# Performance work log

Measured on AMD Instinct MI355X. Metric: run time of the kernel, lower is better.

## Reference

```python
import jax, jax.numpy as jnp
import numpy as np

B, T, C = 4, 2048, 2048
H = 16
D = C // H  # 128


def setup_inputs() -> dict:
    key = jax.random.key(0)
    k1, k2, k3, k4 = jax.random.split(key, 4)
    x = jax.random.normal(k1, (B, T, C), dtype=jnp.float32)
    rope_freqs = jax.random.uniform(k2, (D // 2,), dtype=jnp.float32)
    # torch Linear weights: (out_features, in_features)
    W_attn = jax.random.normal(k3, (3 * C, C), dtype=jnp.float32) * (1.0 / np.sqrt(C))
    W_proj = jax.random.normal(k4, (C, C), dtype=jnp.float32) * (1.0 / np.sqrt(C))
    return {"x": x, "rope_freqs": rope_freqs, "W_attn": W_attn, "W_proj": W_proj}


def _apply_rope(q, k, rope_freqs):
    # q, k: (B, H, T, D); rope_freqs: (D//2,)
    S = q.shape[2]
    positions = jnp.arange(S, dtype=q.dtype)[:, None]            # (S, 1)
    theta = positions * rope_freqs[None, :]                       # (S, D//2)
    sin_t = jnp.sin(theta)[None, None]                            # (1,1,S,D//2)
    cos_t = jnp.cos(theta)[None, None]
    q1, q2 = q[..., 0::2], q[..., 1::2]
    k1, k2 = k[..., 0::2], k[..., 1::2]
    q_out = jnp.concatenate([q1 * cos_t - q2 * sin_t, q1 * sin_t + q2 * cos_t], axis=-1)
    k_out = jnp.concatenate([k1 * cos_t - k2 * sin_t, k1 * sin_t + k2 * cos_t], axis=-1)
    return q_out, k_out


def reference(x, rope_freqs, W_attn, W_proj):
    b, t, c = x.shape
    qkv = jnp.einsum('btc,fc->btf', x, W_attn)                    # (B,T,3C)
    q, k, v = jnp.split(qkv, 3, axis=-1)
    q = q.reshape(b, t, H, D).transpose(0, 2, 1, 3)               # (B,H,T,D)
    k = k.reshape(b, t, H, D).transpose(0, 2, 1, 3)
    v = v.reshape(b, t, H, D).transpose(0, 2, 1, 3)
    q, k = _apply_rope(q, k, rope_freqs)
    scale = 1.0 / jnp.sqrt(jnp.asarray(D, dtype=x.dtype))
    scores = jnp.einsum('bhqd,bhkd->bhqk', q, k) * scale          # (B,H,T,T)
    causal = jnp.tril(jnp.ones((t, t), dtype=bool))
    scores = jnp.where(causal[None, None], scores, jnp.asarray(-jnp.inf, dtype=scores.dtype))
    probs = jax.nn.softmax(scores, axis=-1)
    y = jnp.einsum('bhqk,bhkd->bhqd', probs, v)                   # (B,H,T,D)
    y = y.transpose(0, 2, 1, 3).reshape(b, t, c)
    return jnp.einsum('btc,fc->btf', y, W_proj)
```

## Files before the change

### kernel.cpp

```cpp
#include <hip/hip_runtime.h>
#include <cstdint>
#include <cstddef>


typedef unsigned short u16;
typedef u16    u16x8 __attribute__((ext_vector_type(8)));
typedef __bf16 bf16x8 __attribute__((ext_vector_type(8)));
typedef float  f32x4 __attribute__((ext_vector_type(4)));

#define MFMA16(a, b, c) __builtin_amdgcn_mfma_f32_16x16x32_bf16( \
    __builtin_bit_cast(bf16x8, (a)), __builtin_bit_cast(bf16x8, (b)), (c), 0, 0, 0)

static __device__ __forceinline__ u16 f2b(float f) {
  unsigned u = __builtin_bit_cast(unsigned, f);
  unsigned r = (u + 0x7FFFu + ((u >> 16) & 1u)) >> 16;
  return (u16)r;
}

static __device__ __forceinline__ void gld_lds16(const void* g, void* l) {
  __builtin_amdgcn_global_load_lds(
      (__attribute__((address_space(1))) unsigned int*)(void*)(g),
      (__attribute__((address_space(3))) unsigned int*)(l),
      16, 0, 0);
}

#define BARRIER() asm volatile("s_barrier" ::: "memory")
#define LGKM0()   do { asm volatile("s_waitcnt lgkmcnt(0)" ::: "memory"); \
                       __builtin_amdgcn_sched_barrier(0); } while (0)
#define WAIT_VM(n) asm volatile("s_waitcnt vmcnt(" #n ")" ::: "memory")

__global__ __launch_bounds__(256) void cvt_bf16(const float4* __restrict__ src,
                                                u16x8* __restrict__ dst, int n8) {
  int i = blockIdx.x * 256 + threadIdx.x;
  if (i >= n8) return;
  float4 a = src[i * 2], b = src[i * 2 + 1];
  u16x8 o;
  o[0] = f2b(a.x); o[1] = f2b(a.y); o[2] = f2b(a.z); o[3] = f2b(a.w);
  o[4] = f2b(b.x); o[5] = f2b(b.y); o[6] = f2b(b.z); o[7] = f2b(b.w);
  dst[i] = o;
}

static __device__ __forceinline__ void rdA(u16x8 (&af)[4][2], const u16* p,
                                           int cx0, int cx1) {
#pragma unroll
  for (int i = 0; i < 4; ++i) {
    af[i][0] = *(const u16x8*)(p + i * 1024 + cx0);
    af[i][1] = *(const u16x8*)(p + i * 1024 + cx1);
  }
}

static __device__ __forceinline__ void rdB(u16x8 (&bf)[2][2], const u16* p,
                                           int cx0, int cx1) {
#pragma unroll
  for (int j = 0; j < 2; ++j) {
    bf[j][0] = *(const u16x8*)(p + j * 1024 + cx0);
    bf[j][1] = *(const u16x8*)(p + j * 1024 + cx1);
  }
}

static __device__ __forceinline__ void mm16(f32x4 (&acc)[8][4], int ib, int jb,
                                            const u16x8 (&af)[4][2],
                                            const u16x8 (&bf)[2][2]) {
#pragma unroll
  for (int i = 0; i < 4; ++i)
#pragma unroll
    for (int j = 0; j < 2; ++j) {
      acc[ib + i][jb + j] = MFMA16(af[i][0], bf[j][0], acc[ib + i][jb + j]);
      acc[ib + i][jb + j] = MFMA16(af[i][1], bf[j][1], acc[ib + i][jb + j]);
    }
}

static __device__ __forceinline__ void gemm256_main(
    const u16* __restrict__ A, const u16* __restrict__ Bw, int K,
    int m0, int n0, u16* sm, f32x4 (&acc)[8][4]) {
  const int tid = threadIdx.x;
  const int lane = tid & 63, wv = tid >> 6;
  const int quad = lane >> 4, col = lane & 15;
  const int wm = wv >> 2, wn = wv & 3;

  u16* LA0 = sm;
  u16* LB0 = sm + 16384;
  u16* LA1 = sm + 32768;
  u16* LB1 = sm + 49152;

#pragma unroll
  for (int i = 0; i < 8; ++i)
#pragma unroll
    for (int j = 0; j < 4; ++j) acc[i][j] = (f32x4){0.f, 0.f, 0.f, 0.f};

  const int r8 = lane >> 3, ch = lane & 7;
  const int sc8 = (ch ^ r8) << 3;
  const u16 *aS[4], *bS[4];
  int dof[4];
#pragma unroll
  for (int u = 0; u < 4; ++u) {
    int row = u * 64 + wv * 8 + r8;
    aS[u] = A + (size_t)(m0 + row) * K + sc8;
    bS[u] = Bw + (size_t)(n0 + row) * K + sc8;
    dof[u] = (u * 64 + wv * 8) * 64;
  }

  const int cx0 = ((quad) ^ (col & 7)) << 3;
  const int cx1 = ((4 | quad) ^ (col & 7)) << 3;
  const int offA = (wm * 128 + col) * 64;
  const int offB = (wn * 64 + col) * 64;

  gld_lds16(bS[0], LB0 + dof[0]); gld_lds16(bS[1], LB0 + dof[1]);
  gld_lds16(bS[2], LB0 + dof[2]); gld_lds16(bS[3], LB0 + dof[3]);
  gld_lds16(aS[0], LA0 + dof[0]); gld_lds16(aS[2], LA0 + dof[2]);
  gld_lds16(aS[1], LA0 + dof[1]); gld_lds16(aS[3], LA0 + dof[3]);
  WAIT_VM(2);
  BARRIER();

  u16x8 af[4][2], bfL[2][2], bfH[2][2];
  const int nIt = K >> 7;
#pragma unroll 1
  for (int it = 0; it < nIt; ++it) {
    const size_t ko = (size_t)it * 128 + 64;
    const size_t kn = (size_t)it * 128 + 128;
    const bool hn = (it + 1 < nIt);

    rdA(af, LA0 + offA, cx0, cx1);
    rdB(bfL, LB0 + offB, cx0, cx1);
    gld_lds16(bS[0] + ko, LB1 + dof[0]); gld_lds16(bS[1] + ko, LB1 + dof[1]);
    BARRIER(); LGKM0();
    __builtin_amdgcn_s_setprio(1); mm16(acc, 0, 0, af, bfL);
    __builtin_amdgcn_s_setprio(0);
    BARRIER();
    rdB(bfH, LB0 + offB + 2048, cx0, cx1);
    gld_lds16(bS[2] + ko, LB1 + dof[2]); gld_lds16(bS[3] + ko, LB1 + dof[3]);
    WAIT_VM(4);
    BARRIER(); LGKM0();
    __builtin_amdgcn_s_setprio(1); mm16(acc, 0, 2, af, bfH);
    __builtin_amdgcn_s_setprio(0);
    BARRIER();
    rdA(af, LA0 + offA + 4096, cx0, cx1);
    gld_lds16(aS[0] + ko, LA1 + dof[0]); gld_lds16(aS[2] + ko, LA1 + dof[2]);
    BARRIER(); LGKM0();
    __builtin_amdgcn_s_setprio(1); mm16(acc, 4, 0, af, bfL);
    __builtin_amdgcn_s_setprio(0);
    BARRIER();
    gld_lds16(aS[1] + ko, LA1 + dof[1]); gld_lds16(aS[3] + ko, LA1 + dof[3]);
    WAIT_VM(2);
    BARRIER(); __builtin_amdgcn_sched_barrier(0);
    __builtin_amdgcn_s_setprio(1); mm16(acc, 4, 2, af, bfH);
    __builtin_amdgcn_s_setprio(0);
    BARRIER();
    rdA(af, LA1 + offA, cx0, cx1);
    rdB(bfL, LB1 + offB, cx0, cx1);
    if (hn) { gld_lds16(bS[0] + kn, LB0 + dof[0]); gld_lds16(bS[1] + kn, LB0 + dof[1]); }
    BARRIER(); LGKM0();
    __builtin_amdgcn_s_setprio(1); mm16(acc, 0, 0, af, bfL);
    __builtin_amdgcn_s_setprio(0);
    BARRIER();
    rdB(bfH, LB1 + offB + 2048, cx0, cx1);
    if (hn) {
      gld_lds16(bS[2] + kn, LB0 + dof[2]); gld_lds16(bS[3] + kn, LB0 + dof[3]);
      WAIT_VM(4);
    } else {
      WAIT_VM(0);
    }
    BARRIER(); LGKM0();
    __builtin_amdgcn_s_setprio(1); mm16(acc, 0, 2, af, bfH);
    __builtin_amdgcn_s_setprio(0);
    BARRIER();
    rdA(af, LA1 + offA + 4096, cx0, cx1);
    if (hn) { gld_lds16(aS[0] + kn, LA0 + dof[0]); gld_lds16(aS[2] + kn, LA0 + dof[2]); }
    BARRIER(); LGKM0();
    __builtin_amdgcn_s_setprio(1); mm16(acc, 4, 0, af, bfL);
    __builtin_amdgcn_s_setprio(0);
    BARRIER();
    if (hn) { gld_lds16(aS[1] + kn, LA0 + dof[1]); gld_lds16(aS[3] + kn, LA0 + dof[3]); }
    WAIT_VM(2);
    BARRIER(); __builtin_amdgcn_sched_barrier(0);
    __builtin_amdgcn_s_setprio(1); mm16(acc, 4, 2, af, bfH);
    __builtin_amdgcn_s_setprio(0);
    BARRIER();
  }
}

__global__ __launch_bounds__(512, 2) void gemm_qkv(
    const u16* __restrict__ A, const u16* __restrict__ Bw,
    const float* __restrict__ freqs, int K,
    u16* __restrict__ Qp, u16* __restrict__ Kp, u16* __restrict__ Vp) {
  extern __shared__ u16 sm[];
  const int bid = blockIdx.x;
  const int x = bid & 7, o = bid >> 3;
  const int rnd = o >> 5, w = o & 31;
  const int m0 = (x * 4 + (w & 3)) * 256;
  const int n0 = (rnd * 8 + (w >> 2)) * 256;

  f32x4 acc[8][4];
  gemm256_main(A, Bw, K, m0, n0, sm, acc);

  const int tid = threadIdx.x;
  const int lane = tid & 63, wv = tid >> 6;
  const int quad = lane >> 4, col = lane & 15;
  const int wm = wv >> 2, wn = wv & 3;

  const int which = n0 >> 11;
  const int h0 = (n0 & 2047) >> 7;
  const int b = m0 >> 11, t0 = m0 & 2047;
  const int hl = wn >> 1;


  if (which == 2) {
#pragma unroll
    for (int j = 0; j < 4; ++j) {
      int d = (wn & 1) * 64 + j * 16 + col;
      int key = (d >> 1) & 7;
#pragma unroll
      for (int i = 0; i < 8; ++i) {
        int tbase = wm * 128 + i * 16 + quad * 4;
        int reg = hl * 4 + (tbase >> 6);
        int tc0 = tbase & 63;
        u16* d0 = sm + reg * 8192 + d * 64 + ((((tc0 >> 3) ^ key)) << 3) + (tc0 & 7);
        *(unsigned*)d0 = (unsigned)f2b(acc[i][j][0]) |
                         ((unsigned)f2b(acc[i][j][1]) << 16);
        *(unsigned*)(d0 + 2) = (unsigned)f2b(acc[i][j][2]) |
                               ((unsigned)f2b(acc[i][j][3]) << 16);
      }
    }
    __syncthreads();
#pragma unroll
    for (int s = 0; s < 16; ++s) {
      int cch = tid + (s << 9);
      int reg = cch >> 10, ci = cch & 1023;
      int d = ci >> 3, cc = ci & 7;
      u16x8 v = *(const u16x8*)(sm + reg * 8192 + d * 64 +
                                (((cc ^ ((d >> 1) & 7))) << 3));
      int hh = reg >> 2, ktg = reg & 3;
      int kt = (t0 >> 6) + ktg;
      size_t off = (((size_t)((b * 16 + h0 + hh) * 32 + kt)) << 13) +
                   (size_t)d * 64 + (cc << 3);
      *(u16x8*)(Vp + off) = v;
    }
  } else {
    u16* dst = (which == 0) ? Qp : Kp;
    const bool evenlane = (col & 1) == 0;
    const int rlo = evenlane ? 0 : 2;
#pragma unroll
    for (int j = 0; j < 4; ++j) {
      int dd = (wn & 1) * 64 + j * 16 + col;
      int jj = dd >> 1;
      float fr = freqs[jj];
#pragma unroll
      for (int i = 0; i < 8; ++i) {
        float oth[4];
#pragma unroll
        for (int r = 0; r < 4; ++r) oth[r] = __shfl_xor(acc[i][j][r], 1);
#pragma unroll
        for (int rr = 0; rr < 2; ++rr) {
          int r = rlo + rr;
          float q1 = evenlane ? acc[i][j][r] : oth[r];
          float q2 = evenlane ? oth[r] : acc[i][j][r];
          int tgl = wm * 128 + i * 16 + quad * 4 + r;
          int t = t0 + tgl;
          float theta = (float)t * fr;
          float rev = theta * 0.15915494309189535f;
          rev -= floorf(rev);
          float sn = __builtin_amdgcn_sinf(rev);
          float cs = __builtin_amdgcn_cosf(rev);
          unsigned pk = (unsigned)f2b(q1 * cs - q2 * sn) |
                        ((unsigned)f2b(q1 * sn + q2 * cs) << 16);
          int row = hl * 256 + tgl;
          int sc = (jj >> 2) ^ (row & 15);
          *(unsigned*)(sm + row * 128 + (sc << 3) + 2 * (jj & 3)) = pk;
        }
      }
    }
    __syncthreads();
#pragma unroll
    for (int s = 0; s < 16; ++s) {
      int cch = tid + (s << 9);
      int row = cch >> 4, cc = cch & 15;
      u16x8 v = *(const u16x8*)(sm + row * 128 + ((cc ^ (row & 15)) << 3));
      int hh = row >> 8, tl = row & 255;
      size_t off = ((size_t)((b * 16 + h0 + hh) * 2048 + t0 + tl)) * 128 +
                   (cc << 3);
      *(u16x8*)(dst + off) = v;
    }
  }
}

__global__ __launch_bounds__(512, 2) void gemm_proj(
    const u16* __restrict__ A, const u16* __restrict__ Bw,
    int N, int K, float* __restrict__ out) {
  extern __shared__ u16 sm[];
  const int m0 = blockIdx.y * 256, n0 = blockIdx.x * 256;

  f32x4 acc[8][4];
  gemm256_main(A, Bw, K, m0, n0, sm, acc);

  const int tid = threadIdx.x;
  const int lane = tid & 63, wv = tid >> 6;
  const int quad = lane >> 4, col = lane & 15;
  const int wm = wv >> 2, wn = wv & 3;

#pragma unroll
  for (int i = 0; i < 8; ++i) {
    int mg = m0 + wm * 128 + i * 16 + quad * 4;
#pragma unroll
    for (int j = 0; j < 4; ++j) {
      int ng = n0 + wn * 64 + j * 16 + col;
#pragma unroll
      for (int r = 0; r < 4; ++r) out[(size_t)(mg + r) * N + ng] = acc[i][j][r];
    }
  }
}

__global__ __launch_bounds__(512, 4) void fattn(
    const u16* __restrict__ Qb, const u16* __restrict__ Kb, const u16* __restrict__ Vt,
    u16* __restrict__ Yb) {
  __shared__ alignas(16) u16 lK[64 * 128];
  __shared__ alignas(16) u16 lVt[128 * 64];
  __shared__ alignas(16) u16 lP[8][16 * 64];

  const int tid = threadIdx.x;
  const int lane = tid & 63, wv = tid >> 6;
  const int quad = lane >> 4, col = lane & 15;
  const int bh = blockIdx.x;
  const int p = blockIdx.y;
  const int b = bh >> 4, h = bh & 15;
  const size_t base = (size_t)bh << 18;
  const float kcomb = 0.08838834764831845f * 1.4426950408889634f;

#pragma unroll 1
  for (int phase = 0; phase < 2; ++phase) {
    const int tq = phase ? (15 - p) : p;
    const int qr0 = tq * 128 + wv * 16;
    const int dkt = qr0 >> 6;

    u16x8 qf[4];
#pragma unroll
    for (int t = 0; t < 4; ++t)
      qf[t] = *(const u16x8*)(Qb + base + (size_t)(qr0 + col) * 128 + t * 32 + quad * 8);

    f32x4 mrow = (f32x4){-1e30f, -1e30f, -1e30f, -1e30f};
    f32x4 lrow = (f32x4){0.f, 0.f, 0.f, 0.f};
    f32x4 o[8];
#pragma unroll
    for (int dt = 0; dt < 8; ++dt) o[dt] = (f32x4){0.f, 0.f, 0.f, 0.f};

    const int nkt = 2 * tq + 2;
#pragma unroll 1
    for (int kt = 0; kt < nkt; ++kt) {
      __syncthreads();
      if (wv < 4) {
#pragma unroll
        for (int u = 0; u < 4; ++u) {
          int row = wv * 16 + u * 4 + (lane >> 4);
          int sc = (lane & 15) ^ (row & 15);
          gld_lds16(Kb + base + (size_t)(kt * 64 + row) * 128 + (sc << 3),
                    lK + (size_t)(wv * 16 + u * 4) * 128);
        }
      } else {
        int vw = wv - 4;
        const u16* vbase = Vt + ((size_t)(bh * 32 + kt) << 13);
#pragma unroll
        for (int u = 0; u < 4; ++u) {
          int row = vw * 32 + u * 8 + (lane >> 3);
          int sc = (lane & 7) ^ (row & 7);
          gld_lds16(vbase + (size_t)row * 64 + (sc << 3),
                    lVt + (size_t)(vw * 32 + u * 8) * 64);
        }
      }
      __syncthreads();

      if (kt <= dkt) {
        f32x4 sv[4];
#pragma unroll
        for (int nt = 0; nt < 4; ++nt) {
          f32x4 s = (f32x4){0.f, 0.f, 0.f, 0.f};
#pragma unroll
          for (int t = 0; t < 4; ++t) {
            int krow = nt * 16 + col;
            u16x8 kf = *(const u16x8*)&lK[krow * 128 + ((((t << 2) | quad) ^ (krow & 15)) << 3)];
            s = MFMA16(qf[t], kf, s);
          }
          sv[nt] = s;
        }
#pragma unroll
        for (int nt = 0; nt < 4; ++nt)
#pragma unroll
          for (int r = 0; r < 4; ++r) sv[nt][r] *= kcomb;
        if (kt == dkt) {
#pragma unroll
          for (int nt = 0; nt < 4; ++nt) {
            int cg = kt * 64 + nt * 16 + col;
#pragma unroll
            for (int r = 0; r < 4; ++r)
              if (cg > qr0 + quad * 4 + r) sv[nt][r] = -1e30f;
          }
        }
        f32x4 mx = sv[0];
#pragma unroll
        for (int nt = 1; nt < 4; ++nt)
#pragma unroll
          for (int r = 0; r < 4; ++r) mx[r] = fmaxf(mx[r], sv[nt][r]);
#pragma unroll
        for (int off = 1; off < 16; off <<= 1)
#pragma unroll
          for (int r = 0; r < 4; ++r) mx[r] = fmaxf(mx[r], __shfl_xor(mx[r], off));
        f32x4 alpha;
#pragma unroll
        for (int r = 0; r < 4; ++r) {
          float mn = fmaxf(mrow[r], mx[r]);
          alpha[r] = exp2f(mrow[r] - mn);
          mrow[r] = mn;
        }
        f32x4 ps = (f32x4){0.f, 0.f, 0.f, 0.f};
#pragma unroll
        for (int nt = 0; nt < 4; ++nt)
#pragma unroll
          for (int r = 0; r < 4; ++r) {
            float pe = exp2f(sv[nt][r] - mrow[r]);
            ps[r] += pe;
            int row = quad * 4 + r;
            int ch = ((nt << 1) | (col >> 3)) ^ (row & 7);
            lP[wv][row * 64 + (ch << 3) + (col & 7)] = f2b(pe);
          }
#pragma unroll
        for (int off = 1; off < 16; off <<= 1)
#pragma unroll
          for (int r = 0; r < 4; ++r) ps[r] += __shfl_xor(ps[r], off);
#pragma unroll
        for (int r = 0; r < 4; ++r) lrow[r] = lrow[r] * alpha[r] + ps[r];
#pragma unroll
        for (int dt = 0; dt < 8; ++dt)
#pragma unroll
          for (int r = 0; r < 4; ++r) o[dt][r] *= alpha[r];
#pragma unroll
        for (int t = 0; t < 2; ++t) {
          u16x8 pf = *(const u16x8*)&lP[wv][col * 64 + ((((t << 2) | quad) ^ (col & 7)) << 3)];
#pragma unroll
          for (int dt = 0; dt < 8; ++dt) {
            int drow = dt * 16 + col;
            u16x8 vf = *(const u16x8*)&lVt[drow * 64 + ((((t << 2) | quad) ^ (drow & 7)) << 3)];
            o[dt] = MFMA16(pf, vf, o[dt]);
          }
        }
      }
    }

    f32x4 inv;
#pragma unroll
    for (int r = 0; r < 4; ++r) inv[r] = 1.0f / lrow[r];
#pragma unroll
    for (int dt = 0; dt < 8; ++dt)
#pragma unroll
      for (int r = 0; r < 4; ++r) {
        float y = o[dt][r] * inv[r];
        int q = qr0 + quad * 4 + r;
        Yb[((size_t)(b * 2048 + q)) * 2048 + h * 128 + dt * 16 + col] = f2b(y);
      }
  }
}

extern "C" void kernel_launch(void* const* d_in, const int* in_sizes, int n_in,
                              void* d_out, int out_size, void* d_ws, size_t ws_size,
                              hipStream_t stream) {
  (void)in_sizes; (void)n_in; (void)out_size; (void)ws_size;
  const float* x     = (const float*)d_in[0];
  const float* freqs = (const float*)d_in[1];
  const float* Wattn = (const float*)d_in[2];
  const float* Wproj = (const float*)d_in[3];
  float* out = (float*)d_out;
  char* ws = (char*)d_ws;

  u16* Wq_b = (u16*)(ws + 0);
  u16* Wp_b = (u16*)(ws + 25165824);
  u16* x_b  = (u16*)(ws + 33554432);
  u16* Qb   = (u16*)(ws + 67108864);
  u16* Kb   = (u16*)(ws + 100663296);
  u16* Vt   = (u16*)(ws + 134217728);
  u16* Yb   = (u16*)(ws + 167772160);

  static bool attr_done = false;
  if (!attr_done) {
    (void)hipFuncSetAttribute((const void*)gemm_qkv,
                              hipFuncAttributeMaxDynamicSharedMemorySize, 131072);
    (void)hipFuncSetAttribute((const void*)gemm_proj,
                              hipFuncAttributeMaxDynamicSharedMemorySize, 131072);
    attr_done = true;
  }

  cvt_bf16<<<6144, 256, 0, stream>>>((const float4*)Wattn, (u16x8*)Wq_b, 12582912 / 8);
  cvt_bf16<<<2048, 256, 0, stream>>>((const float4*)Wproj, (u16x8*)Wp_b, 4194304 / 8);
  cvt_bf16<<<8192, 256, 0, stream>>>((const float4*)x, (u16x8*)x_b, 16777216 / 8);

  gemm_qkv<<<dim3(768), 512, 131072, stream>>>(x_b, Wq_b, freqs, 2048, Qb, Kb, Vt);
  fattn<<<dim3(64, 8), 512, 0, stream>>>(Qb, Kb, Vt, Yb);
  gemm_proj<<<dim3(8, 32), 512, 131072, stream>>>(Yb, Wp_b, 2048, 2048, out);
}
```

Measured before the change: 591.6 us.

## Load GEMM B operand directly from global into registers, drop B LDS staging

```diff
diff --git a/kernel.cpp b/kernel.cpp
--- a/kernel.cpp
+++ b/kernel.cpp
@@ -49,24 +49,25 @@
   }
 }
 
-static __device__ __forceinline__ void rdB(u16x8 (&bf)[2][2], const u16* p,
-                                           int cx0, int cx1) {
-#pragma unroll
-  for (int j = 0; j < 2; ++j) {
-    bf[j][0] = *(const u16x8*)(p + j * 1024 + cx0);
-    bf[j][1] = *(const u16x8*)(p + j * 1024 + cx1);
-  }
-}
-
-static __device__ __forceinline__ void mm16(f32x4 (&acc)[8][4], int ib, int jb,
+static __device__ __forceinline__ void ldB(u16x8 (&bf)[4][2],
+                                           const u16* const (&bp)[4],
+                                           size_t k0) {
+#pragma unroll
+  for (int j = 0; j < 4; ++j) {
+    bf[j][0] = *(const u16x8*)(bp[j] + k0);
+    bf[j][1] = *(const u16x8*)(bp[j] + k0 + 32);
+  }
+}
+
+static __device__ __forceinline__ void mm32(f32x4 (&acc)[8][4], int ib,
                                             const u16x8 (&af)[4][2],
-                                            const u16x8 (&bf)[2][2]) {
+                                            const u16x8 (&bf)[4][2]) {
 #pragma unroll
   for (int i = 0; i < 4; ++i)
 #pragma unroll
-    for (int j = 0; j < 2; ++j) {
-      acc[ib + i][jb + j] = MFMA16(af[i][0], bf[j][0], acc[ib + i][jb + j]);
-      acc[ib + i][jb + j] = MFMA16(af[i][1], bf[j][1], acc[ib + i][jb + j]);
+    for (int j = 0; j < 4; ++j) {
+      acc[ib + i][j] = MFMA16(af[i][0], bf[j][0], acc[ib + i][j]);
+      acc[ib + i][j] = MFMA16(af[i][1], bf[j][1], acc[ib + i][j]);
     }
 }
 
@@ -79,9 +80,7 @@
   const int wm = wv >> 2, wn = wv & 3;
 
   u16* LA0 = sm;
-  u16* LB0 = sm + 16384;
-  u16* LA1 = sm + 32768;
-  u16* LB1 = sm + 49152;
+  u16* LA1 = sm + 16384;
 
 #pragma unroll
   for (int i = 0; i < 8; ++i)
@@ -90,29 +89,32 @@
 
   const int r8 = lane >> 3, ch = lane & 7;
   const int sc8 = (ch ^ r8) << 3;
-  const u16 *aS[4], *bS[4];
+  const u16* aS[4];
   int dof[4];
 #pragma unroll
   for (int u = 0; u < 4; ++u) {
     int row = u * 64 + wv * 8 + r8;
     aS[u] = A + (size_t)(m0 + row) * K + sc8;
-    bS[u] = Bw + (size_t)(n0 + row) * K + sc8;
     dof[u] = (u * 64 + wv * 8) * 64;
   }
+
+  const u16* bp[4];
+#pragma unroll
+  for (int j = 0; j < 4; ++j)
+    bp[j] = Bw + (size_t)(n0 + wn * 64 + j * 16 + col) * K + quad * 8;
 
   const int cx0 = ((quad) ^ (col & 7)) << 3;
   const int cx1 = ((4 | quad) ^ (col & 7)) << 3;
   const int offA = (wm * 128 + col) * 64;
-  const int offB = (wn * 64 + col) * 64;
-
-  gld_lds16(bS[0], LB0 + dof[0]); gld_lds16(bS[1], LB0 + dof[1]);
-  gld_lds16(bS[2], LB0 + dof[2]); gld_lds16(bS[3], LB0 + dof[3]);
-  gld_lds16(aS[0], LA0 + dof[0]); gld_lds16(aS[2], LA0 + dof[2]);
-  gld_lds16(aS[1], LA0 + dof[1]); gld_lds16(aS[3], LA0 + dof[3]);
-  WAIT_VM(2);
+
+  u16x8 af[4][2], bfE[4][2], bfO[4][2];
+
+  gld_lds16(aS[0], LA0 + dof[0]); gld_lds16(aS[1], LA0 + dof[1]);
+  gld_lds16(aS[2], LA0 + dof[2]); gld_lds16(aS[3], LA0 + dof[3]);
+  ldB(bfE, bp, 0);
+  WAIT_VM(0);
   BARRIER();
 
-  u16x8 af[4][2], bfL[2][2], bfH[2][2];
   const int nIt = K >> 7;
 #pragma unroll 1
   for (int it = 0; it < nIt; ++it) {
@@ -120,61 +122,34 @@
     const size_t kn = (size_t)it * 128 + 128;
     const bool hn = (it + 1 < nIt);
 
+    gld_lds16(aS[0] + ko, LA1 + dof[0]); gld_lds16(aS[1] + ko, LA1 + dof[1]);
+    gld_lds16(aS[2] + ko, LA1 + dof[2]); gld_lds16(aS[3] + ko, LA1 + dof[3]);
+    ldB(bfO, bp, ko);
     rdA(af, LA0 + offA, cx0, cx1);
-    rdB(bfL, LB0 + offB, cx0, cx1);
-    gld_lds16(bS[0] + ko, LB1 + dof[0]); gld_lds16(bS[1] + ko, LB1 + dof[1]);
-    BARRIER(); LGKM0();
-    __builtin_amdgcn_s_setprio(1); mm16(acc, 0, 0, af, bfL);
+    LGKM0();
+    __builtin_amdgcn_s_setprio(1); mm32(acc, 0, af, bfE);
     __builtin_amdgcn_s_setprio(0);
+    rdA(af, LA0 + offA + 4096, cx0, cx1);
+    LGKM0();
+    __builtin_amdgcn_s_setprio(1); mm32(acc, 4, af, bfE);
+    __builtin_amdgcn_s_setprio(0);
+    WAIT_VM(0);
     BARRIER();
-    rdB(bfH, LB0 + offB + 2048, cx0, cx1);
-    gld_lds16(bS[2] + ko, LB1 + dof[2]); gld_lds16(bS[3] + ko, LB1 + dof[3]);
-    WAIT_VM(4);
-    BARRIER(); LGKM0();
-    __builtin_amdgcn_s_setprio(1); mm16(acc, 0, 2, af, bfH);
+
+    if (hn) {
+      gld_lds16(aS[0] + kn, LA0 + dof[0]); gld_lds16(aS[1] + kn, LA0 + dof[1]);
+      gld_lds16(aS[2] + kn, LA0 + dof[2]); gld_lds16(aS[3] + kn, LA0 + dof[3]);
+      ldB(bfE, bp, kn);
+    }
+    rdA(af, LA1 + offA, cx0, cx1);
+    LGKM0();
+    __builtin_amdgcn_s_setprio(1); mm32(acc, 0, af, bfO);
     __builtin_amdgcn_s_setprio(0);
-    BARRIER();
-    rdA(af, LA0 + offA + 4096, cx0, cx1);
-    gld_lds16(aS[0] + ko, LA1 + dof[0]); gld_lds16(aS[2] + ko, LA1 + dof[2]);
-    BARRIER(); LGKM0();
-    __builtin_amdgcn_s_setprio(1); mm16(acc, 4, 0, af, bfL);
+    rdA(af, LA1 + offA + 4096, cx0, cx1);
+    LGKM0();
+    __builtin_amdgcn_s_setprio(1); mm32(acc, 4, af, bfO);
     __builtin_amdgcn_s_setprio(0);
-    BARRIER();
-    gld_lds16(aS[1] + ko, LA1 + dof[1]); gld_lds16(aS[3] + ko, LA1 + dof[3]);
-    WAIT_VM(2);
-    BARRIER(); __builtin_amdgcn_sched_barrier(0);
-    __builtin_amdgcn_s_setprio(1); mm16(acc, 4, 2, af, bfH);
-    __builtin_amdgcn_s_setprio(0);
-    BARRIER();
-    rdA(af, LA1 + offA, cx0, cx1);
-    rdB(bfL, LB1 + offB, cx0, cx1);
-    if (hn) { gld_lds16(bS[0] + kn, LB0 + dof[0]); gld_lds16(bS[1] + kn, LB0 + dof[1]); }
-    BARRIER(); LGKM0();
-    __builtin_amdgcn_s_setprio(1); mm16(acc, 0, 0, af, bfL);
-    __builtin_amdgcn_s_setprio(0);
-    BARRIER();
-    rdB(bfH, LB1 + offB + 2048, cx0, cx1);
-    if (hn) {
-      gld_lds16(bS[2] + kn, LB0 + dof[2]); gld_lds16(bS[3] + kn, LB0 + dof[3]);
-      WAIT_VM(4);
-    } else {
-      WAIT_VM(0);
-    }
-    BARRIER(); LGKM0();
-    __builtin_amdgcn_s_setprio(1); mm16(acc, 0, 2, af, bfH);
-    __builtin_amdgcn_s_setprio(0);
-    BARRIER();
-    rdA(af, LA1 + offA + 4096, cx0, cx1);
-    if (hn) { gld_lds16(aS[0] + kn, LA0 + dof[0]); gld_lds16(aS[2] + kn, LA0 + dof[2]); }
-    BARRIER(); LGKM0();
-    __builtin_amdgcn_s_setprio(1); mm16(acc, 4, 0, af, bfL);
-    __builtin_amdgcn_s_setprio(0);
-    BARRIER();
-    if (hn) { gld_lds16(aS[1] + kn, LA0 + dof[1]); gld_lds16(aS[3] + kn, LA0 + dof[3]); }
-    WAIT_VM(2);
-    BARRIER(); __builtin_amdgcn_sched_barrier(0);
-    __builtin_amdgcn_s_setprio(1); mm16(acc, 4, 2, af, bfH);
-    __builtin_amdgcn_s_setprio(0);
+    WAIT_VM(0);
     BARRIER();
   }
 }
```

Result: slower. 783.5 us (+32.4%).
